# Optimization experiments

Measured on AMD Instinct MI355X. Metric: run time of the kernel, lower is better.

Reference implementation:

```python
import jax, jax.numpy as jnp
import numpy as np

B, N, C, H, D = 1, 4096, 256, 8, 64  # batch, seq, channels, heads, head_dim


def setup_inputs() -> dict:
    key = jax.random.key(0)
    ks = jax.random.split(key, 11)
    s = 0.02
    return {
        "q_x": jax.random.normal(ks[0], (B, N, C), jnp.float32),
        "k_x": jax.random.normal(ks[1], (B, N, C), jnp.float32),
        "v_x": jax.random.normal(ks[2], (B, N, C), jnp.float32),
        "bias": jax.random.normal(ks[3], (B, 1, N, N), jnp.float32),
        "wq": jax.random.normal(ks[4], (H * D, C), jnp.float32) * s,
        "wk": jax.random.normal(ks[5], (H * D, C), jnp.float32) * s,
        "wv": jax.random.normal(ks[6], (H * D, C), jnp.float32) * s,
        "wg": jax.random.normal(ks[7], (H * D, C), jnp.float32) * s,
        "bg": jnp.ones((H * D,), jnp.float32),  # gating bias init = 1
        "wo": jax.random.normal(ks[8], (C, H * D), jnp.float32) * s,
        "bo": jnp.zeros((C,), jnp.float32),
        "q_chunk_size": 256,
        "kv_chunk_size": 1024,
    }


def reference(q_x, k_x, v_x, bias, wq, wk, wv, wg, bg, wo, bo,
              q_chunk_size, kv_chunk_size):
    # The chunked Rabe-Staats loop computes exact softmax attention; the
    # chunk sizes are memory knobs only, so the reference computes the
    # mathematically identical full attention.
    q = (q_x @ wq.T).reshape(*q_x.shape[:-1], H, D) / jnp.sqrt(jnp.asarray(D, q_x.dtype))
    k = (k_x @ wk.T).reshape(*k_x.shape[:-1], H, D)
    v = (v_x @ wv.T).reshape(*v_x.shape[:-1], H, D)
    logits = jnp.einsum("bqhd,bkhd->bhqk", q, k) + bias  # [B,H,Q,K]
    p = jax.nn.softmax(logits, axis=-1)
    o = jnp.einsum("bkhd,bhqk->bqhd", v, p)  # [B,Q,H,D]
    g = jax.nn.sigmoid(q_x @ wg.T + bg).reshape(*q_x.shape[:-1], H, D)
    o = o * g
    o = o.reshape(*o.shape[:-2], H * D)
    return o @ wo.T + bo
```

## Files before the change

kernel.cpp:

```cpp
#include <hip/hip_runtime.h>
#include <stdint.h>

#define NN 4096
#define CC 256
#define HD 512
#define DD 64
#define KSPLIT 2

typedef __attribute__((ext_vector_type(8))) short short8;
typedef __attribute__((ext_vector_type(4))) float floatx4;

__device__ __forceinline__ unsigned short f2bf(float x) {
    union { float f; unsigned int u; } v; v.f = x;
    unsigned int u = v.u + 0x7fffu + ((v.u >> 16) & 1u);
    return (unsigned short)(u >> 16);
}
__device__ __forceinline__ float bf2f(unsigned short s) {
    union { unsigned int u; float f; } v; v.u = ((unsigned int)s) << 16;
    return v.f;
}

#if defined(__has_builtin) && __has_builtin(__builtin_amdgcn_cvt_pk_bf16_f32)
typedef __attribute__((ext_vector_type(2))) __bf16 bf16x2_t;
__device__ __forceinline__ unsigned int pack2bf(float a, float b) {
    union { bf16x2_t v; unsigned int u; } x;
    x.v = __builtin_amdgcn_cvt_pk_bf16_f32(a, b);
    return x.u;
}
#else
__device__ __forceinline__ unsigned int pack2bf(float a, float b) {
    return ((unsigned int)f2bf(b) << 16) | (unsigned int)f2bf(a);
}
#endif

#define GLOAD_LDS(gp, lp) __builtin_amdgcn_global_load_lds(                    \
    (__attribute__((address_space(1))) void*)(gp),                             \
    (__attribute__((address_space(3))) void*)(lp), 16, 0, 0)

__global__ __launch_bounds__(256) void prep_kernel(
    const float* __restrict__ qx, const float* __restrict__ kx,
    const float* __restrict__ vx,
    const float* __restrict__ wq, const float* __restrict__ wk,
    const float* __restrict__ wv, const float* __restrict__ wg,
    const float* __restrict__ wo,
    unsigned short* __restrict__ qxb, unsigned short* __restrict__ kxb,
    unsigned short* __restrict__ vxb, unsigned short* __restrict__ Wb,
    unsigned short* __restrict__ wob)
{
    const int z = blockIdx.y;
    const float* src; unsigned short* dst; int n; float s = 1.0f;
    switch (z) {
        case 0: src = qx; dst = qxb; n = NN * CC; break;
        case 1: src = kx; dst = kxb; n = NN * CC; break;
        case 2: src = vx; dst = vxb; n = NN * CC; break;
        case 3: src = wq; dst = Wb;               n = HD * CC; s = 0.125f; break;
        case 4: src = wk; dst = Wb + 1 * HD * CC; n = HD * CC; break;
        case 5: src = wv; dst = Wb + 2 * HD * CC; n = HD * CC; break;
        case 6: src = wg; dst = Wb + 3 * HD * CC; n = HD * CC; break;
        default: src = wo; dst = wob;             n = CC * HD; break;
    }
    int i = (blockIdx.x * 256 + threadIdx.x) * 4;
    if (i < n) {
        float4 v = *(const float4*)&src[i];
        ushort4 p;
        p.x = f2bf(v.x * s); p.y = f2bf(v.y * s);
        p.z = f2bf(v.z * s); p.w = f2bf(v.w * s);
        *(ushort4*)&dst[i] = p;
    }
}

__global__ __launch_bounds__(256, 4) void proj_kernel(
    const unsigned short* __restrict__ qxb, const unsigned short* __restrict__ kxb,
    const unsigned short* __restrict__ vxb, const unsigned short* __restrict__ Wb,
    const float* __restrict__ bg,
    unsigned short* __restrict__ Qb, unsigned short* __restrict__ Kb,
    unsigned short* __restrict__ VbT, unsigned short* __restrict__ Gb)
{
    const int m0 = blockIdx.x * 128;
    const int nb = blockIdx.y;
    const int n0 = nb * 128;
    const int mode = nb >> 2;
    const unsigned short* X = (mode == 1) ? kxb : (mode == 2) ? vxb : qxb;

    const int tid = threadIdx.x;
    const int wid = tid >> 6;
    const int wr = wid >> 1, wc = wid & 1;
    const int lane = tid & 63;
    const int quad = lane >> 4;
    const int ln = lane & 15;
    const int lnx = ln & 7;

    __shared__ __align__(16) unsigned short smem[128 * 136];
    unsigned short* Xs = smem;
    unsigned short* Ws = smem + 128 * 64;

    floatx4 acc[4][4] = {};

    for (int k0 = 0; k0 < CC; k0 += 64) {
        #pragma unroll
        for (int t = 0; t < 4; t++) {
            int row = wid * 32 + t * 8 + (lane >> 3);
            int c = (lane & 7) ^ (lane >> 3);
            GLOAD_LDS(&X[(size_t)(m0 + row) * CC + k0 + c * 8],
                      &Xs[(wid * 32 + t * 8) * 64]);
            GLOAD_LDS(&Wb[(size_t)(n0 + row) * CC + k0 + c * 8],
                      &Ws[(wid * 32 + t * 8) * 64]);
        }
        __syncthreads();

        #pragma unroll
        for (int ks = 0; ks < 64; ks += 32) {
            const int cb = ks >> 3;
            short8 a[4], b[4];
            #pragma unroll
            for (int i = 0; i < 4; i++)
                a[i] = *(const short8*)&Xs[(wr * 64 + i * 16 + ln) * 64 +
                                           (((quad ^ cb) ^ lnx) * 8)];
            #pragma unroll
            for (int j = 0; j < 4; j++)
                b[j] = *(const short8*)&Ws[(wc * 64 + j * 16 + ln) * 64 +
                                           (((quad ^ cb) ^ lnx) * 8)];
            #pragma unroll
            for (int i = 0; i < 4; i++)
                #pragma unroll
                for (int j = 0; j < 4; j++)
                    acc[i][j] = __builtin_amdgcn_mfma_f32_16x16x32_bf16(a[i], b[j], acc[i][j], 0, 0, 0);
        }
        __syncthreads();
    }

    const int subn = nb & 3;
    if (mode != 2) {
        unsigned short* Out = (mode == 0) ? Qb : (mode == 1) ? Kb : Gb;
        #pragma unroll
        for (int i = 0; i < 4; i++) {
            #pragma unroll
            for (int j = 0; j < 4; j++) {
                int col = subn * 128 + wc * 64 + j * 16 + ln;
                float bgv = (mode == 3) ? bg[col] : 0.0f;
                #pragma unroll
                for (int r = 0; r < 4; r++) {
                    int row = m0 + wr * 64 + i * 16 + quad * 4 + r;
                    float v = acc[i][j][r];
                    if (mode == 3) v = 1.0f / (1.0f + __expf(-(v + bgv)));
                    Out[(size_t)row * HD + col] = f2bf(v);
                }
            }
        }
    } else {
        #pragma unroll
        for (int i = 0; i < 4; i++) {
            #pragma unroll
            for (int j = 0; j < 4; j++) {
                int cl = wc * 64 + j * 16 + ln;
                #pragma unroll
                for (int r = 0; r < 4; r++) {
                    int rl = wr * 64 + i * 16 + quad * 4 + r;
                    smem[cl * 136 + rl] = f2bf(acc[i][j][r]);
                }
            }
        }
        __syncthreads();
        #pragma unroll
        for (int it = 0; it < 8; it++) {
            int idx = it * 256 + tid;
            int c = idx >> 4, ch = idx & 15;
            short8 vv = *(const short8*)&smem[c * 136 + ch * 8];
            *(short8*)&VbT[(size_t)(subn * 128 + c) * NN + m0 + ch * 8] = vv;
        }
    }
}

__global__ __launch_bounds__(256, 4) void attn_kernel(
    const unsigned short* __restrict__ Qb, const unsigned short* __restrict__ Kb,
    const unsigned short* __restrict__ VbT,
    const float* __restrict__ bias,
    unsigned short* __restrict__ Opart, float* __restrict__ Lpart)
{
    const int h = blockIdx.y;
    const int q0 = blockIdx.x * 64;
    const int sp = blockIdx.z;
    const int tbeg = sp * 32;
    const int tid = threadIdx.x;
    const int wid = tid >> 6;
    const int lane = tid & 63;
    const int quad = lane >> 4;
    const int ln = lane & 15;
    const int lnx = ln & 7;
    const int hi3 = (ln >> 3) << 3;
    const int sc = (lane & 7) ^ (lane >> 3);

    __shared__ __align__(16) unsigned short Ks[2][64 * 64];
    __shared__ __align__(16) unsigned short Vs[2][64 * 64];
    __shared__ __align__(16) unsigned short Ps[64 * 64];

    const int qrow = q0 + wid * 16 + ln;
    short8 qa0 = *(const short8*)&Qb[(size_t)qrow * HD + h * DD + quad * 8];
    short8 qa1 = *(const short8*)&Qb[(size_t)qrow * HD + h * DD + 32 + quad * 8];

    floatx4 O[4] = {};
    float lsum[4] = {0.0f, 0.0f, 0.0f, 0.0f};

    auto STAGE = [&](int kt, int bf) {
        const size_t k0 = (size_t)kt * 64;
        #pragma unroll
        for (int t = 0; t < 2; t++) {
            int row = wid * 16 + t * 8 + (lane >> 3);
            GLOAD_LDS(&Kb[(k0 + row) * HD + h * DD + sc * 8],
                      &Ks[bf][(wid * 16 + t * 8) * 64]);
            GLOAD_LDS(&VbT[(size_t)(h * DD + row) * NN + k0 + sc * 8],
                      &Vs[bf][(wid * 16 + t * 8) * 64]);
        }
    };

    const float* bbase = &bias[(size_t)(q0 + wid * 16 + quad * 4) * NN + ln];
    auto LBIAS = [&](int kt, float (&bv)[4][4]) {
        #pragma unroll
        for (int r = 0; r < 4; r++)
            #pragma unroll
            for (int n = 0; n < 4; n++)
                bv[r][n] = bbase[(size_t)r * NN + kt * 64 + n * 16];
    };

    float bvA[4][4], bvB[4][4];

    STAGE(tbeg, 0);
    LBIAS(tbeg, bvA);
    __syncthreads();

    auto ITER = [&](int kt, int bf, float (&bvC)[4][4], float (&bvN)[4][4],
                    bool pre) {
        if (pre) {
            STAGE(kt + 1, bf ^ 1);
            LBIAS(kt + 1, bvN);
        }

        floatx4 S[4];
        #pragma unroll
        for (int n = 0; n < 4; n++)
            S[n] = (floatx4){bvC[0][n], bvC[1][n], bvC[2][n], bvC[3][n]};
        __builtin_amdgcn_s_setprio(1);
        #pragma unroll
        for (int n = 0; n < 4; n++) {
            short8 b0 = *(const short8*)&Ks[bf][(n * 16 + ln) * 64 + ((quad ^ lnx) * 8)];
            S[n] = __builtin_amdgcn_mfma_f32_16x16x32_bf16(qa0, b0, S[n], 0, 0, 0);
            short8 b1 = *(const short8*)&Ks[bf][(n * 16 + ln) * 64 + (((quad ^ 4) ^ lnx) * 8)];
            S[n] = __builtin_amdgcn_mfma_f32_16x16x32_bf16(qa1, b1, S[n], 0, 0, 0);
        }
        __builtin_amdgcn_s_setprio(0);

        #pragma unroll
        for (int r = 0; r < 4; r++) {
            int prow = wid * 16 + quad * 4 + r;
            int pb = (prow * 64 + lnx) ^ ((prow & 7) << 3) ^ hi3;
            #pragma unroll
            for (int n = 0; n < 4; n += 2) {
                float p0 = __expf(S[n][r]);
                float p1 = __expf(S[n + 1][r]);
                lsum[r] += p0 + p1;
                unsigned int pk = pack2bf(p0, p1);
                Ps[pb ^ (n << 4)] = (unsigned short)(pk & 0xffffu);
                Ps[pb ^ ((n + 1) << 4)] = (unsigned short)(pk >> 16);
            }
        }

        __builtin_amdgcn_s_setprio(1);
        #pragma unroll
        for (int ks = 0; ks < 64; ks += 32) {
            const int cb = ks >> 3;
            short8 a = *(const short8*)&Ps[(wid * 16 + ln) * 64 +
                                           (((cb | quad) ^ lnx) * 8)];
            #pragma unroll
            for (int nd = 0; nd < 4; nd++) {
                short8 vb = *(const short8*)&Vs[bf][(nd * 16 + ln) * 64 +
                                                    (((quad ^ cb) ^ lnx) * 8)];
                O[nd] = __builtin_amdgcn_mfma_f32_16x16x32_bf16(a, vb, O[nd], 0, 0, 0);
            }
        }
        __builtin_amdgcn_s_setprio(0);

        if (pre)
            __syncthreads();
    };

    #pragma unroll 1
    for (int i = 0; i < 30; i += 2) {
        ITER(tbeg + i,     0, bvA, bvB, true);
        ITER(tbeg + i + 1, 1, bvB, bvA, true);
    }
    ITER(tbeg + 30, 0, bvA, bvB, true);
    ITER(tbeg + 31, 1, bvB, bvA, false);

    #pragma unroll
    for (int r = 0; r < 4; r++) {
        #pragma unroll
        for (int off = 1; off < 16; off <<= 1)
            lsum[r] += __shfl_xor(lsum[r], off);
        int grow = q0 + wid * 16 + quad * 4 + r;
        size_t base = ((size_t)(sp * 8 + h) * NN + grow) * 64;
        #pragma unroll
        for (int nd = 0; nd < 4; nd++)
            Opart[base + nd * 16 + ln] = f2bf(O[nd][r]);
        if (ln == 0)
            Lpart[(size_t)(sp * 8 + h) * NN + grow] = lsum[r];
    }
}

__global__ __launch_bounds__(256) void combine_kernel(
    const unsigned short* __restrict__ Opart, const float* __restrict__ Lpart,
    const unsigned short* __restrict__ Gb, unsigned short* __restrict__ OGb)
{
    const int tid = threadIdx.x;
    const int d = tid & 63;
    const int flat = blockIdx.x * 4 + (tid >> 6);
    const int h = flat >> 12;
    const int q = flat & (NN - 1);

    float l = 0.0f, o = 0.0f;
    #pragma unroll
    for (int sp = 0; sp < KSPLIT; sp++) {
        size_t idx = (size_t)(sp * 8 + h) * NN + q;
        l += Lpart[idx];
        o += bf2f(Opart[idx * 64 + d]);
    }
    float inv = 1.0f / l;
    int col = h * DD + d;
    float g = bf2f(Gb[(size_t)q * HD + col]);
    OGb[(size_t)q * HD + col] = f2bf(o * inv * g);
}

__global__ __launch_bounds__(256, 4) void outproj_kernel(
    const unsigned short* __restrict__ OGb, const unsigned short* __restrict__ wob,
    const float* __restrict__ bo, float* __restrict__ out)
{
    const int m0 = blockIdx.x * 64;
    const int n0 = blockIdx.y * 64;
    const int tid = threadIdx.x;
    const int wid = tid >> 6;
    const int lane = tid & 63;
    const int quad = lane >> 4;
    const int ln = lane & 15;
    const int lnx = ln & 7;

    __shared__ __align__(16) unsigned short Xs[64 * 64];
    __shared__ __align__(16) unsigned short Ws[64 * 64];

    floatx4 acc[4] = {};

    for (int k0 = 0; k0 < HD; k0 += 64) {
        #pragma unroll
        for (int t = 0; t < 2; t++) {
            int row = wid * 16 + t * 8 + (lane >> 3);
            int c = (lane & 7) ^ (lane >> 3);
            GLOAD_LDS(&OGb[(size_t)(m0 + row) * HD + k0 + c * 8],
                      &Xs[(wid * 16 + t * 8) * 64]);
            GLOAD_LDS(&wob[(size_t)(n0 + row) * HD + k0 + c * 8],
                      &Ws[(wid * 16 + t * 8) * 64]);
        }
        __syncthreads();

        #pragma unroll
        for (int ks = 0; ks < 64; ks += 32) {
            const int cb = ks >> 3;
            short8 a = *(const short8*)&Xs[(wid * 16 + ln) * 64 +
                                           (((quad ^ cb) ^ lnx) * 8)];
            #pragma unroll
            for (int n = 0; n < 4; n++) {
                short8 b = *(const short8*)&Ws[(n * 16 + ln) * 64 +
                                               (((quad ^ cb) ^ lnx) * 8)];
                acc[n] = __builtin_amdgcn_mfma_f32_16x16x32_bf16(a, b, acc[n], 0, 0, 0);
            }
        }
        __syncthreads();
    }

    #pragma unroll
    for (int n = 0; n < 4; n++) {
        int col = n0 + n * 16 + ln;
        float bov = bo[col];
        #pragma unroll
        for (int r = 0; r < 4; r++) {
            int row = m0 + wid * 16 + quad * 4 + r;
            out[(size_t)row * CC + col] = acc[n][r] + bov;
        }
    }
}

extern "C" void kernel_launch(void* const* d_in, const int* in_sizes, int n_in,
                              void* d_out, int out_size, void* d_ws, size_t ws_size,
                              hipStream_t stream) {
    const float* qx   = (const float*)d_in[0];
    const float* kx   = (const float*)d_in[1];
    const float* vx   = (const float*)d_in[2];
    const float* bias = (const float*)d_in[3];
    const float* wq   = (const float*)d_in[4];
    const float* wk   = (const float*)d_in[5];
    const float* wv   = (const float*)d_in[6];
    const float* wg   = (const float*)d_in[7];
    const float* bg   = (const float*)d_in[8];
    const float* wo   = (const float*)d_in[9];
    const float* bo   = (const float*)d_in[10];
    float* out = (float*)d_out;

    char* ws = (char*)d_ws;
    const size_t MB = (size_t)1 << 20;
    unsigned short* wob   = (unsigned short*)(ws);
    float*          Lpart = (float*)(ws + MB / 4);
    unsigned short* Qb    = (unsigned short*)(ws + 1 * MB);
    unsigned short* Kb    = (unsigned short*)(ws + 5 * MB);
    unsigned short* VbT   = (unsigned short*)(ws + 9 * MB);
    unsigned short* Gb    = (unsigned short*)(ws + 13 * MB);
    unsigned short* OGb   = (unsigned short*)(ws + 17 * MB);
    unsigned short* qxb   = (unsigned short*)(ws + 21 * MB);
    unsigned short* kxb   = (unsigned short*)(ws + 23 * MB);
    unsigned short* vxb   = (unsigned short*)(ws + 25 * MB);
    unsigned short* Wb    = (unsigned short*)(ws + 27 * MB);
    unsigned short* Opart = (unsigned short*)(ws + 21 * MB);

    prep_kernel<<<dim3(NN * CC / (256 * 4), 8), 256, 0, stream>>>(
        qx, kx, vx, wq, wk, wv, wg, wo, qxb, kxb, vxb, Wb, wob);
    proj_kernel<<<dim3(32, 16), 256, 0, stream>>>(
        qxb, kxb, vxb, Wb, bg, Qb, Kb, VbT, Gb);
    attn_kernel<<<dim3(64, 8, KSPLIT), 256, 0, stream>>>(
        Qb, Kb, VbT, bias, Opart, Lpart);
    combine_kernel<<<dim3(NN * 8 / 4), 256, 0, stream>>>(
        Opart, Lpart, Gb, OGb);
    outproj_kernel<<<dim3(64, 4), 256, 0, stream>>>(
        OGb, wob, bo, out);
}
```

Before: 214.4 us.

## Double query tile per block to reuse K/V tiles, split KV three ways

The attention kernel now processes 128 query rows per block (two 16-row MFMA tiles per wave), so each K and V tile staged in LDS feeds twice as much work. The KV split goes from 2 to 3 to keep enough blocks in flight (32x8x3 grid), with uneven tile ranges per split. Bias prefetch now loads straight into the score accumulators after the softmax step, and the hand-unrolled ping-pong loop becomes a generic loop. Costs are more registers, a larger P buffer in LDS, lower occupancy (launch bounds 4 to 3) and a combine step that reads an extra partial.

```diff
diff --git a/kernel.cpp b/kernel.cpp
--- a/kernel.cpp
+++ b/kernel.cpp
@@ -5,7 +5,7 @@
 #define CC 256
 #define HD 512
 #define DD 64
-#define KSPLIT 2
+#define KSPLIT 3
 
 typedef __attribute__((ext_vector_type(8))) short short8;
 typedef __attribute__((ext_vector_type(4))) float floatx4;
@@ -171,16 +171,17 @@
     }
 }
 
-__global__ __launch_bounds__(256, 4) void attn_kernel(
+__global__ __launch_bounds__(256, 3) void attn_kernel(
     const unsigned short* __restrict__ Qb, const unsigned short* __restrict__ Kb,
     const unsigned short* __restrict__ VbT,
     const float* __restrict__ bias,
     unsigned short* __restrict__ Opart, float* __restrict__ Lpart)
 {
     const int h = blockIdx.y;
-    const int q0 = blockIdx.x * 64;
+    const int q0 = blockIdx.x * 128;
     const int sp = blockIdx.z;
-    const int tbeg = sp * 32;
+    const int tbeg = (sp * 64) / KSPLIT;
+    const int tend = ((sp + 1) * 64) / KSPLIT;
     const int tid = threadIdx.x;
     const int wid = tid >> 6;
     const int lane = tid & 63;
@@ -192,14 +193,19 @@
 
     __shared__ __align__(16) unsigned short Ks[2][64 * 64];
     __shared__ __align__(16) unsigned short Vs[2][64 * 64];
-    __shared__ __align__(16) unsigned short Ps[64 * 64];
-
-    const int qrow = q0 + wid * 16 + ln;
-    short8 qa0 = *(const short8*)&Qb[(size_t)qrow * HD + h * DD + quad * 8];
-    short8 qa1 = *(const short8*)&Qb[(size_t)qrow * HD + h * DD + 32 + quad * 8];
-
-    floatx4 O[4] = {};
-    float lsum[4] = {0.0f, 0.0f, 0.0f, 0.0f};
+    __shared__ __align__(16) unsigned short Ps[128 * 64];
+
+    short8 qa[2][2];
+    #pragma unroll
+    for (int m = 0; m < 2; m++) {
+        const int qrow = q0 + wid * 32 + m * 16 + ln;
+        qa[m][0] = *(const short8*)&Qb[(size_t)qrow * HD + h * DD + quad * 8];
+        qa[m][1] = *(const short8*)&Qb[(size_t)qrow * HD + h * DD + 32 + quad * 8];
+    }
+
+    floatx4 O[2][4] = {};
+    floatx4 S[2][4];
+    float lsum[2][4] = {};
 
     auto STAGE = [&](int kt, int bf) {
         const size_t k0 = (size_t)kt * 64;
@@ -213,96 +219,97 @@
         }
     };
 
-    const float* bbase = &bias[(size_t)(q0 + wid * 16 + quad * 4) * NN + ln];
-    auto LBIAS = [&](int kt, float (&bv)[4][4]) {
-        #pragma unroll
-        for (int r = 0; r < 4; r++)
+    const float* bbase = &bias[(size_t)(q0 + wid * 32 + quad * 4) * NN + ln];
+    auto LBIAS_S = [&](int kt) {
+        #pragma unroll
+        for (int m = 0; m < 2; m++)
             #pragma unroll
             for (int n = 0; n < 4; n++)
-                bv[r][n] = bbase[(size_t)r * NN + kt * 64 + n * 16];
+                #pragma unroll
+                for (int r = 0; r < 4; r++)
+                    S[m][n][r] = bbase[(size_t)(m * 16 + r) * NN + kt * 64 + n * 16];
     };
 
-    float bvA[4][4], bvB[4][4];
-
     STAGE(tbeg, 0);
-    LBIAS(tbeg, bvA);
+    LBIAS_S(tbeg);
     __syncthreads();
 
-    auto ITER = [&](int kt, int bf, float (&bvC)[4][4], float (&bvN)[4][4],
-                    bool pre) {
-        if (pre) {
-            STAGE(kt + 1, bf ^ 1);
-            LBIAS(kt + 1, bvN);
-        }
-
-        floatx4 S[4];
-        #pragma unroll
-        for (int n = 0; n < 4; n++)
-            S[n] = (floatx4){bvC[0][n], bvC[1][n], bvC[2][n], bvC[3][n]};
+    #pragma unroll 1
+    for (int kt = tbeg; kt < tend; ++kt) {
+        const int bf = (kt - tbeg) & 1;
+        const bool pre = (kt + 1 < tend);
+
+        if (pre) STAGE(kt + 1, bf ^ 1);
+
         __builtin_amdgcn_s_setprio(1);
         #pragma unroll
         for (int n = 0; n < 4; n++) {
             short8 b0 = *(const short8*)&Ks[bf][(n * 16 + ln) * 64 + ((quad ^ lnx) * 8)];
-            S[n] = __builtin_amdgcn_mfma_f32_16x16x32_bf16(qa0, b0, S[n], 0, 0, 0);
+            S[0][n] = __builtin_amdgcn_mfma_f32_16x16x32_bf16(qa[0][0], b0, S[0][n], 0, 0, 0);
+            S[1][n] = __builtin_amdgcn_mfma_f32_16x16x32_bf16(qa[1][0], b0, S[1][n], 0, 0, 0);
             short8 b1 = *(const short8*)&Ks[bf][(n * 16 + ln) * 64 + (((quad ^ 4) ^ lnx) * 8)];
-            S[n] = __builtin_amdgcn_mfma_f32_16x16x32_bf16(qa1, b1, S[n], 0, 0, 0);
+            S[0][n] = __builtin_amdgcn_mfma_f32_16x16x32_bf16(qa[0][1], b1, S[0][n], 0, 0, 0);
+            S[1][n] = __builtin_amdgcn_mfma_f32_16x16x32_bf16(qa[1][1], b1, S[1][n], 0, 0, 0);
         }
         __builtin_amdgcn_s_setprio(0);
 
         #pragma unroll
-        for (int r = 0; r < 4; r++) {
-            int prow = wid * 16 + quad * 4 + r;
-            int pb = (prow * 64 + lnx) ^ ((prow & 7) << 3) ^ hi3;
-            #pragma unroll
-            for (int n = 0; n < 4; n += 2) {
-                float p0 = __expf(S[n][r]);
-                float p1 = __expf(S[n + 1][r]);
-                lsum[r] += p0 + p1;
-                unsigned int pk = pack2bf(p0, p1);
-                Ps[pb ^ (n << 4)] = (unsigned short)(pk & 0xffffu);
-                Ps[pb ^ ((n + 1) << 4)] = (unsigned short)(pk >> 16);
+        for (int m = 0; m < 2; m++) {
+            #pragma unroll
+            for (int r = 0; r < 4; r++) {
+                int prow = wid * 32 + m * 16 + quad * 4 + r;
+                int pb = (prow * 64 + lnx) ^ ((prow & 7) << 3) ^ hi3;
+                #pragma unroll
+                for (int n = 0; n < 4; n += 2) {
+                    float p0 = __expf(S[m][n][r]);
+                    float p1 = __expf(S[m][n + 1][r]);
+                    lsum[m][r] += p0 + p1;
+                    unsigned int pk = pack2bf(p0, p1);
+                    Ps[pb ^ (n << 4)] = (unsigned short)(pk & 0xffffu);
+                    Ps[pb ^ ((n + 1) << 4)] = (unsigned short)(pk >> 16);
+                }
             }
         }
+
+        if (pre) LBIAS_S(kt + 1);
 
         __builtin_amdgcn_s_setprio(1);
         #pragma unroll
         for (int ks = 0; ks < 64; ks += 32) {
             const int cb = ks >> 3;
-            short8 a = *(const short8*)&Ps[(wid * 16 + ln) * 64 +
-                                           (((cb | quad) ^ lnx) * 8)];
+            short8 a0 = *(const short8*)&Ps[(wid * 32 + ln) * 64 +
+                                            (((cb | quad) ^ lnx) * 8)];
+            short8 a1 = *(const short8*)&Ps[(wid * 32 + 16 + ln) * 64 +
+                                            (((cb | quad) ^ lnx) * 8)];
             #pragma unroll
             for (int nd = 0; nd < 4; nd++) {
                 short8 vb = *(const short8*)&Vs[bf][(nd * 16 + ln) * 64 +
                                                     (((quad ^ cb) ^ lnx) * 8)];
-                O[nd] = __builtin_amdgcn_mfma_f32_16x16x32_bf16(a, vb, O[nd], 0, 0, 0);
+                O[0][nd] = __builtin_amdgcn_mfma_f32_16x16x32_bf16(a0, vb, O[0][nd], 0, 0, 0);
+                O[1][nd] = __builtin_amdgcn_mfma_f32_16x16x32_bf16(a1, vb, O[1][nd], 0, 0, 0);
             }
         }
         __builtin_amdgcn_s_setprio(0);
 
         if (pre)
             __syncthreads();
-    };
-
-    #pragma unroll 1
-    for (int i = 0; i < 30; i += 2) {
-        ITER(tbeg + i,     0, bvA, bvB, true);
-        ITER(tbeg + i + 1, 1, bvB, bvA, true);
-    }
-    ITER(tbeg + 30, 0, bvA, bvB, true);
-    ITER(tbeg + 31, 1, bvB, bvA, false);
+    }
 
     #pragma unroll
-    for (int r = 0; r < 4; r++) {
-        #pragma unroll
-        for (int off = 1; off < 16; off <<= 1)
-            lsum[r] += __shfl_xor(lsum[r], off);
-        int grow = q0 + wid * 16 + quad * 4 + r;
-        size_t base = ((size_t)(sp * 8 + h) * NN + grow) * 64;
-        #pragma unroll
-        for (int nd = 0; nd < 4; nd++)
-            Opart[base + nd * 16 + ln] = f2bf(O[nd][r]);
-        if (ln == 0)
-            Lpart[(size_t)(sp * 8 + h) * NN + grow] = lsum[r];
+    for (int m = 0; m < 2; m++) {
+        #pragma unroll
+        for (int r = 0; r < 4; r++) {
+            #pragma unroll
+            for (int off = 1; off < 16; off <<= 1)
+                lsum[m][r] += __shfl_xor(lsum[m][r], off);
+            int grow = q0 + wid * 32 + m * 16 + quad * 4 + r;
+            size_t base = ((size_t)(sp * 8 + h) * NN + grow) * 64;
+            #pragma unroll
+            for (int nd = 0; nd < 4; nd++)
+                Opart[base + nd * 16 + ln] = f2bf(O[m][nd][r]);
+            if (ln == 0)
+                Lpart[(size_t)(sp * 8 + h) * NN + grow] = lsum[m][r];
+        }
     }
 }
 
@@ -421,7 +428,7 @@
         qx, kx, vx, wq, wk, wv, wg, wo, qxb, kxb, vxb, Wb, wob);
     proj_kernel<<<dim3(32, 16), 256, 0, stream>>>(
         qxb, kxb, vxb, Wb, bg, Qb, Kb, VbT, Gb);
-    attn_kernel<<<dim3(64, 8, KSPLIT), 256, 0, stream>>>(
+    attn_kernel<<<dim3(32, 8, KSPLIT), 256, 0, stream>>>(
         Qb, Kb, VbT, bias, Opart, Lpart);
     combine_kernel<<<dim3(NN * 8 / 4), 256, 0, stream>>>(
         Opart, Lpart, Gb, OGb);
```

Measured after the change: 237.0 us. 1.11x slower.
